# Kernel tuning notes

Hardware: AMD Instinct MI355X
Metric: run time of the kernel (lower is better)

The kernel has to match this reference:

```python
import jax, jax.numpy as jnp
import numpy as np

N = 8192
IN_FEAT = 256
OUT_FEAT = 128
SLOPE = 0.1
NEG_INF = -9e15


def setup_inputs() -> dict:
    key = jax.random.key(0)
    k_doc, k_Ww, k_Wb, k_aw, k_ab = jax.random.split(key, 5)
    doc = jax.random.normal(k_doc, (N, IN_FEAT), dtype=jnp.float32)
    # nn.Linear(inFeat, outFeat): weight [out, in], bias [out]
    W_w = jax.random.normal(k_Ww, (OUT_FEAT, IN_FEAT), dtype=jnp.float32) / np.sqrt(IN_FEAT)
    W_b = jax.random.normal(k_Wb, (OUT_FEAT,), dtype=jnp.float32) * 0.01
    # nn.Linear(2*outFeat, 1): weight [1, 2*out], bias [1]
    a_w = jax.random.normal(k_aw, (1, 2 * OUT_FEAT), dtype=jnp.float32) / np.sqrt(2 * OUT_FEAT)
    a_b = jax.random.normal(k_ab, (1,), dtype=jnp.float32) * 0.01
    return {"doc": doc, "W_w": W_w, "W_b": W_b, "a_w": a_w, "a_b": a_b, "selfLink": 0}


def reference(doc, W_w, W_b, a_w, a_b, selfLink):
    # h = W(doc)  -> [N, outFeat]
    h = doc @ W_w.T + W_b
    n = h.shape[0]
    # Original builds fch[i, j] = concat(h_i, h_j) -> [N, N, 2D] and applies
    # Linear(2D, 1). Algebraically: score[i,j] = h_i . a_src + h_j . a_dst + b,
    # where a_src/a_dst are the two halves of the weight. Same math, O(N*D) mem.
    a_src = a_w[0, :OUT_FEAT]   # [D]
    a_dst = a_w[0, OUT_FEAT:]   # [D]
    s_src = h @ a_src           # [N]
    s_dst = h @ a_dst           # [N]
    att = jax.nn.leaky_relu(s_src[:, None] + s_dst[None, :] + a_b[0], SLOPE)  # [N, N]
    if selfLink == 0:
        # adj = 1 - eye: mask self-edges
        diag = jnp.eye(n, dtype=bool)
        att = jnp.where(diag, NEG_INF, att)
    att = jax.nn.softmax(att, axis=1)
    h_out = jax.nn.leaky_relu(att @ h, SLOPE)  # [N, D]
    return (h_out, att)
```

## Files before the change

kernel.cpp:

```cpp
#include <hip/hip_runtime.h>
#include <math.h>

#define NROW 8192
#define IN_F 256
#define OUT_F 128
#define SLOPE 0.1f
#define SEGS 256
#define SEGROWS 32

typedef float f32x4 __attribute__((ext_vector_type(4)));

__device__ __forceinline__ float lrelu(float x) { return x > 0.f ? x : SLOPE * x; }

__global__ __launch_bounds__(256) void kA_h_s(const float* __restrict__ doc,
                                              const float* __restrict__ Ww,
                                              const float* __restrict__ Wb,
                                              const float* __restrict__ aw,
                                              float* __restrict__ h,
                                              float* __restrict__ s_src,
                                              float* __restrict__ s_dst,
                                              float* __restrict__ E1,
                                              float* __restrict__ E2) {
    __shared__ float4 sdoc[16][64];
    const int t = threadIdx.x;
    const int rowBase = blockIdx.x * 16;
    const float4* doc4 = (const float4*)(doc + (size_t)rowBase * IN_F);
    float4* sflat = &sdoc[0][0];
    for (int i = t; i < 16 * 64; i += 256) sflat[i] = doc4[i];
    __syncthreads();
    const int cq = t & 31;
    const int rg = t >> 5;
    const float4* w0 = (const float4*)(Ww + (size_t)(4 * cq + 0) * IN_F);
    const float4* w1 = (const float4*)(Ww + (size_t)(4 * cq + 1) * IN_F);
    const float4* w2 = (const float4*)(Ww + (size_t)(4 * cq + 2) * IN_F);
    const float4* w3 = (const float4*)(Ww + (size_t)(4 * cq + 3) * IN_F);
    float a00 = 0.f, a01 = 0.f, a02 = 0.f, a03 = 0.f;
    float a10 = 0.f, a11 = 0.f, a12 = 0.f, a13 = 0.f;
#pragma unroll 4
    for (int k = 0; k < 64; ++k) {
        const float4 d0 = sdoc[2 * rg + 0][k];
        const float4 d1 = sdoc[2 * rg + 1][k];
        float4 w;
        w = w0[k];
        a00 += d0.x * w.x + d0.y * w.y + d0.z * w.z + d0.w * w.w;
        a10 += d1.x * w.x + d1.y * w.y + d1.z * w.z + d1.w * w.w;
        w = w1[k];
        a01 += d0.x * w.x + d0.y * w.y + d0.z * w.z + d0.w * w.w;
        a11 += d1.x * w.x + d1.y * w.y + d1.z * w.z + d1.w * w.w;
        w = w2[k];
        a02 += d0.x * w.x + d0.y * w.y + d0.z * w.z + d0.w * w.w;
        a12 += d1.x * w.x + d1.y * w.y + d1.z * w.z + d1.w * w.w;
        w = w3[k];
        a03 += d0.x * w.x + d0.y * w.y + d0.z * w.z + d0.w * w.w;
        a13 += d1.x * w.x + d1.y * w.y + d1.z * w.z + d1.w * w.w;
    }
    const float4 wb4 = ((const float4*)Wb)[cq];
    const float4 as4 = ((const float4*)aw)[cq];
    const float4 ad4 = ((const float4*)(aw + OUT_F))[cq];

#define KA_EPILOG(A0, A1, A2, A3, RR)                                           \
    do {                                                                        \
        float4 hv;                                                              \
        hv.x = (A0) + wb4.x; hv.y = (A1) + wb4.y;                               \
        hv.z = (A2) + wb4.z; hv.w = (A3) + wb4.w;                               \
        const int row = rowBase + 2 * rg + (RR);                                \
        ((float4*)(h + (size_t)row * OUT_F))[cq] = hv;                          \
        float ps = hv.x * as4.x + hv.y * as4.y + hv.z * as4.z + hv.w * as4.w;   \
        float pd = hv.x * ad4.x + hv.y * ad4.y + hv.z * ad4.z + hv.w * ad4.w;   \
        for (int off = 16; off; off >>= 1) {                                    \
            ps += __shfl_down(ps, off, 32);                                     \
            pd += __shfl_down(pd, off, 32);                                     \
        }                                                                       \
        if (cq == 0) {                                                          \
            s_src[row] = ps;                                                    \
            s_dst[row] = pd;                                                    \
            E1[row] = expf(pd);                                                 \
            E2[row] = expf(SLOPE * pd);                                         \
        }                                                                       \
    } while (0)

    KA_EPILOG(a00, a01, a02, a03, 0);
    KA_EPILOG(a10, a11, a12, a13, 1);
#undef KA_EPILOG
}

__global__ __launch_bounds__(256) void kBC_rank_top2(const float* __restrict__ sdst,
                                                     float* __restrict__ red,
                                                     int* __restrict__ perm) {
    const int t = threadIdx.x;
    if (blockIdx.x == SEGS) {
        float m1 = -1e30f, m2 = -1e30f; int i1 = 0;
        for (int j = t; j < NROW; j += 256) {
            const float v = sdst[j];
            if (v > m1) { m2 = m1; m1 = v; i1 = j; }
            else if (v > m2) { m2 = v; }
        }
        __shared__ float sm1[256], sm2[256];
        __shared__ int si[256];
        sm1[t] = m1; sm2[t] = m2; si[t] = i1;
        __syncthreads();
        for (int s = 128; s > 0; s >>= 1) {
            if (t < s) {
                const float om1 = sm1[t + s], om2 = sm2[t + s];
                const int oi = si[t + s];
                if (om1 > sm1[t]) {
                    sm2[t] = fmaxf(sm1[t], om2);
                    sm1[t] = om1; si[t] = oi;
                } else {
                    sm2[t] = fmaxf(sm2[t], om1);
                }
            }
            __syncthreads();
        }
        if (t == 0) { red[0] = sm1[0]; red[1] = sm2[0]; red[2] = __int_as_float(si[0]); }
    } else {
        __shared__ float sd[NROW];
        {
            float4* sd4 = (float4*)sd;
            const float4* g4 = (const float4*)sdst;
            for (int q = t; q < NROW / 4; q += 256) sd4[q] = g4[q];
        }
        __syncthreads();
        const int wave = t >> 6, lane = t & 63;
        const int base = blockIdx.x * 32 + wave * 8;
        float rv[8]; int ri[8]; int cnt[8];
#pragma unroll
        for (int r = 0; r < 8; ++r) { ri[r] = base + r; rv[r] = sd[ri[r]]; cnt[r] = 0; }
        for (int j = lane; j < NROW; j += 64) {
            const float v = sd[j];
#pragma unroll
            for (int r = 0; r < 8; ++r)
                cnt[r] += (v < rv[r] || (v == rv[r] && j < ri[r])) ? 1 : 0;
        }
#pragma unroll
        for (int r = 0; r < 8; ++r)
            for (int off = 32; off; off >>= 1) cnt[r] += __shfl_down(cnt[r], off);
        if (lane == 0) {
#pragma unroll
            for (int r = 0; r < 8; ++r) perm[cnt[r]] = ri[r];
        }
    }
}

__global__ __launch_bounds__(256) void kD_gseg(const int* __restrict__ perm,
                                               const float* __restrict__ E1,
                                               const float* __restrict__ E2,
                                               const float* __restrict__ sdst,
                                               const float* __restrict__ h,
                                               float* __restrict__ sortedS,
                                               float* __restrict__ E1s,
                                               float* __restrict__ E2s,
                                               float* __restrict__ seg1,
                                               float* __restrict__ seg2) {
    __shared__ int sp[SEGROWS];
    __shared__ float se1[SEGROWS], se2[SEGROWS];
    __shared__ float part[2][OUT_F][2];
    const int t = threadIdx.x;
    const int s = blockIdx.x;
    const int r0 = s * SEGROWS;
    if (t < SEGROWS) {
        const int i = perm[r0 + t];
        sp[t] = i;
        const float e1 = E1[i], e2 = E2[i];
        se1[t] = e1; se2[t] = e2;
        sortedS[r0 + t] = sdst[i];
        E1s[r0 + t] = e1;
        E2s[r0 + t] = e2;
    }
    __syncthreads();
    const int c = t & 127;
    const int half = t >> 7;
    float a1 = 0.f, a2 = 0.f;
#pragma unroll
    for (int rr2 = 0; rr2 < 16; ++rr2) {
        const int rr = half * 16 + rr2;
        const float hv = h[(size_t)sp[rr] * OUT_F + c];
        a1 += se1[rr] * hv;
        a2 += se2[rr] * hv;
    }
    part[half][c][0] = a1;
    part[half][c][1] = a2;
    __syncthreads();
    if (t < 128) {
        seg1[(size_t)s * OUT_F + t] = part[0][t][0] + part[1][t][0];
    } else {
        const int c2 = t - 128;
        seg2[(size_t)s * OUT_F + c2] = part[0][c2][1] + part[1][c2][1];
    }
}

__global__ __launch_bounds__(256) void kE_scan(const float* __restrict__ seg1,
                                               const float* __restrict__ seg2,
                                               const float* __restrict__ E1s,
                                               const float* __restrict__ E2s,
                                               float* __restrict__ segUo,
                                               float* __restrict__ segVo,
                                               float* __restrict__ Psuf,
                                               float* __restrict__ Qpre) {
    const int p = blockIdx.x;
    const int t = threadIdx.x;
    if (p < 256) {
        const int arr = p >> 7;
        const int col = p & 127;
        const float* src = arr ? seg2 : seg1;
        const float x = src[(size_t)t * OUT_F + col];
        __shared__ float buf[256];
        const int j = arr ? t : (255 - t);
        buf[j] = x;
        __syncthreads();
        for (int off = 1; off < 256; off <<= 1) {
            const float add = (j >= off) ? buf[j - off] : 0.f;
            __syncthreads();
            buf[j] += add;
            __syncthreads();
        }
        const float excl = buf[j] - x;
        float* dst = arr ? segVo : segUo;
        dst[(size_t)t * OUT_F + col] = excl;
    } else if (p == 256) {
        __shared__ float pp[256];
        const int r0 = t * 32;
        float a = 0.f;
        for (int rr = 0; rr < 32; ++rr) a += E1s[r0 + rr];
        pp[t] = a;
        __syncthreads();
        float off = 0.f;
        for (int t2 = t + 1; t2 < 256; ++t2) off += pp[t2];
        float run = off;
        for (int rr = 31; rr >= 0; --rr) { run += E1s[r0 + rr]; Psuf[r0 + rr] = run; }
        if (t == 0) Psuf[NROW] = 0.f;
    } else {
        __shared__ float pp[256];
        const int r0 = t * 32;
        float a = 0.f;
        for (int rr = 0; rr < 32; ++rr) a += E2s[r0 + rr];
        pp[t] = a;
        __syncthreads();
        float off = 0.f;
        for (int t2 = 0; t2 < t; ++t2) off += pp[t2];
        float rv = off;
        for (int rr = 0; rr < 32; ++rr) { Qpre[r0 + rr] = rv; rv += E2s[r0 + rr]; }
        if (t == 255) Qpre[NROW] = rv;
    }
}

__global__ __launch_bounds__(256) void kF_uv(const int* __restrict__ perm,
                                             const float* __restrict__ h,
                                             const float* __restrict__ E1s,
                                             const float* __restrict__ E2s,
                                             const float* __restrict__ segUo,
                                             const float* __restrict__ segVo,
                                             float* __restrict__ U,
                                             float* __restrict__ V) {
    __shared__ int sp[SEGROWS];
    __shared__ float se1[SEGROWS], se2[SEGROWS];
    __shared__ float sUo[OUT_F], sVo[OUT_F];
    const int t = threadIdx.x;
    const int s = blockIdx.x;
    const int r0 = s * SEGROWS;
    if (t < 128) sUo[t] = segUo[(size_t)s * OUT_F + t];
    else         sVo[t - 128] = segVo[(size_t)s * OUT_F + (t - 128)];
    if (t < SEGROWS) {
        sp[t] = perm[r0 + t];
        se1[t] = E1s[r0 + t];
        se2[t] = E2s[r0 + t];
    }
    __syncthreads();
    const int c = t & 127;
    const int doV = t >> 7;
    float xv[SEGROWS];
#pragma unroll
    for (int rr = 0; rr < SEGROWS; ++rr)
        xv[rr] = h[(size_t)sp[rr] * OUT_F + c];
    if (!doV) {
        float run = sUo[c];
#pragma unroll
        for (int rr = SEGROWS - 1; rr >= 0; --rr) {
            run += se1[rr] * xv[rr];
            U[(size_t)(r0 + rr) * OUT_F + c] = run;
        }
        if (s == SEGS - 1) U[(size_t)NROW * OUT_F + c] = 0.f;
    } else {
        float rv = sVo[c];
#pragma unroll
        for (int rr = 0; rr < SEGROWS; ++rr) {
            V[(size_t)(r0 + rr) * OUT_F + c] = rv;
            rv += se2[rr] * xv[rr];
        }
        if (s == SEGS - 1) V[(size_t)NROW * OUT_F + c] = rv;
    }
}

__global__ __launch_bounds__(256) void kG_hout(const float* __restrict__ s_src,
                                               const float* __restrict__ sdst,
                                               const float* __restrict__ sortedS,
                                               const float* __restrict__ Psuf,
                                               const float* __restrict__ Qpre,
                                               const float* __restrict__ red,
                                               const float* __restrict__ ab,
                                               const int* __restrict__ selfLink,
                                               const float* __restrict__ U,
                                               const float* __restrict__ V,
                                               const float* __restrict__ h,
                                               float* __restrict__ A,
                                               float* __restrict__ B,
                                               float* __restrict__ rZ,
                                               float* __restrict__ T,
                                               float* __restrict__ hout) {
    const int t = threadIdx.x;
    const int i = blockIdx.x * 2 + (t >> 7);
    const int c = t & 127;
    const bool mask = (selfLink[0] == 0);
    const float tt = s_src[i] + ab[0];
    const float M1 = red[0], M2 = red[1];
    const int i1 = __float_as_int(red[2]);
    const float M = (mask && i1 == i) ? M2 : M1;
    const float m = lrelu(tt + M);
    const float Ai = expf(tt - m);
    const float Bi = expf(SLOPE * tt - m);
    const float eii = mask ? expf(lrelu(tt + sdst[i]) - m) : 0.f;
    const float thr = -tt;
    int lo = 0, hi = NROW;
    while (lo < hi) {
        const int mid = (lo + hi) >> 1;
        if (sortedS[mid] > thr) hi = mid; else lo = mid + 1;
    }
    const int k = lo;
    const float Z = Ai * Psuf[k] + Bi * Qpre[k] - eii;
    const float rZi = 1.f / Z;
    const float val = Ai * U[(size_t)k * OUT_F + c] + Bi * V[(size_t)k * OUT_F + c]
                    - eii * h[(size_t)i * OUT_F + c];
    hout[(size_t)i * OUT_F + c] = lrelu(val * rZi);
    if (c == 0) { A[i] = Ai; B[i] = Bi; rZ[i] = rZi; T[i] = tt; }
}

#define RH 16
__global__ __launch_bounds__(256) void kH_att(const float* __restrict__ sdst,
                                              const float* __restrict__ E1,
                                              const float* __restrict__ E2,
                                              const float* __restrict__ A,
                                              const float* __restrict__ B,
                                              const float* __restrict__ rZ,
                                              const float* __restrict__ T,
                                              const int* __restrict__ selfLink,
                                              float* __restrict__ att) {
    __shared__ float rA[RH], rB[RH], rT[RH];
    const int t = threadIdx.x;
    const int rowBase = blockIdx.x * RH;
    if (t < RH) {
        const int i = rowBase + t;
        const float z = rZ[i];
        rA[t] = A[i] * z;
        rB[t] = B[i] * z;
        rT[t] = -T[i];
    }
    __syncthreads();
    const bool mask = (selfLink[0] == 0);
    const f32x4* s4p = (const f32x4*)sdst;
    const f32x4* e1p = (const f32x4*)E1;
    const f32x4* e2p = (const f32x4*)E2;
    for (int it = 0; it < NROW / (4 * 256); ++it) {
        const int q = it * 256 + t;
        const f32x4 s4 = s4p[q];
        const f32x4 e1 = e1p[q];
        const f32x4 e2 = e2p[q];
        const int j0 = q * 4;
#pragma unroll
        for (int r = 0; r < RH; ++r) {
            const float a = rA[r], b = rB[r], thr = rT[r];
            f32x4 o;
            o.x = s4.x > thr ? a * e1.x : b * e2.x;
            o.y = s4.y > thr ? a * e1.y : b * e2.y;
            o.z = s4.z > thr ? a * e1.z : b * e2.z;
            o.w = s4.w > thr ? a * e1.w : b * e2.w;
            const int i = rowBase + r;
            const int d = i - j0;
            if (mask && ((unsigned)d < 4u)) {
                if (d == 0) o.x = 0.f;
                else if (d == 1) o.y = 0.f;
                else if (d == 2) o.z = 0.f;
                else o.w = 0.f;
            }
            __builtin_nontemporal_store(o, (f32x4*)(att + (size_t)i * NROW) + q);
        }
    }
}

extern "C" void kernel_launch(void* const* d_in, const int* in_sizes, int n_in,
                              void* d_out, int out_size, void* d_ws, size_t ws_size,
                              hipStream_t stream) {
    const float* doc = (const float*)d_in[0];
    const float* Ww  = (const float*)d_in[1];
    const float* Wb  = (const float*)d_in[2];
    const float* aw  = (const float*)d_in[3];
    const float* ab  = (const float*)d_in[4];
    const int* selfLink = (const int*)d_in[5];

    float* out  = (float*)d_out;
    float* hout = out;
    float* att  = out + (size_t)NROW * OUT_F;

    float* h = att;
    float* U = att + 1048576;
    float* V = att + 1048576 + 1048704;

    float* ws = (float*)d_ws;
    float* s_src   = ws;
    float* s_dst   = ws + 8192;
    float* E1      = ws + 16384;
    float* E2      = ws + 24576;
    float* sortedS = ws + 32768;
    float* E1s     = ws + 40960;
    float* E2s     = ws + 49152;
    float* Aarr    = ws + 57344;
    float* Barr    = ws + 65536;
    float* rZ      = ws + 73728;
    float* Tarr    = ws + 81920;
    int*   perm    = (int*)(ws + 90112);
    float* seg1    = ws + 98304;
    float* seg2    = ws + 131072;
    float* segUo   = ws + 163840;
    float* segVo   = ws + 196608;
    float* Psuf    = ws + 229376;
    float* Qpre    = ws + 237632;
    float* red     = ws + 245888;

    kA_h_s       <<<512,  256, 0, stream>>>(doc, Ww, Wb, aw, h, s_src, s_dst, E1, E2);
    kBC_rank_top2<<<257,  256, 0, stream>>>(s_dst, red, perm);
    kD_gseg      <<<256,  256, 0, stream>>>(perm, E1, E2, s_dst, h, sortedS, E1s, E2s, seg1, seg2);
    kE_scan      <<<258,  256, 0, stream>>>(seg1, seg2, E1s, E2s, segUo, segVo, Psuf, Qpre);
    kF_uv        <<<256,  256, 0, stream>>>(perm, h, E1s, E2s, segUo, segVo, U, V);
    kG_hout      <<<4096, 256, 0, stream>>>(s_src, s_dst, sortedS, Psuf, Qpre, red, ab, selfLink,
                                            U, V, h, Aarr, Barr, rZ, Tarr, hout);
    kH_att       <<<512,  256, 0, stream>>>(s_dst, E1, E2, Aarr, Barr, rZ, Tarr, selfLink, att);
}
```

Measured before the change: 426.0 us.

## Fuse hout and attention-write kernels, moving h/U/V scratch into workspace

Adds a fused kernel that computes each 16-row block's softmax scalars once (binary search over sortedS staged in shared memory), writes hout, and then streams the attention rows. h, U and V move from the att output buffer into the workspace when it is large enough, so the fused kernel does not overwrite its own inputs. The att stores also drop from nontemporal to ordinary stores. This saves one launch and the A/B/rZ/T round trip, at the cost of a 32KB shared-memory copy per block. The fused path runs only if ws_size is big enough.

Result: faster. 415.3 us (-2.5%).

```diff
diff --git a/kernel.cpp b/kernel.cpp
--- a/kernel.cpp
+++ b/kernel.cpp
@@ -291,6 +291,106 @@
     }
 }
 
+#define RH 16
+__global__ __launch_bounds__(256) void kGH_hout_att(const float* __restrict__ s_src,
+                                                    const float* __restrict__ sdst,
+                                                    const float* __restrict__ sortedS,
+                                                    const float* __restrict__ Psuf,
+                                                    const float* __restrict__ Qpre,
+                                                    const float* __restrict__ red,
+                                                    const float* __restrict__ ab,
+                                                    const int* __restrict__ selfLink,
+                                                    const float* __restrict__ U,
+                                                    const float* __restrict__ V,
+                                                    const float* __restrict__ h,
+                                                    const float* __restrict__ E1,
+                                                    const float* __restrict__ E2,
+                                                    float* __restrict__ hout,
+                                                    float* __restrict__ att) {
+    __shared__ float sS[NROW];
+    __shared__ float sAi[RH], sBi[RH], srZ[RH], seii[RH];
+    __shared__ int   sk[RH];
+    __shared__ float rA[RH], rB[RH], rT[RH];
+    const int t = threadIdx.x;
+    const int rowBase = blockIdx.x * RH;
+    {
+        f32x4* d = (f32x4*)sS;
+        const f32x4* s = (const f32x4*)sortedS;
+        for (int q = t; q < NROW / 4; q += 256) d[q] = s[q];
+    }
+    __syncthreads();
+    if (t < RH) {
+        const int i = rowBase + t;
+        const bool mask = (selfLink[0] == 0);
+        const float tt = s_src[i] + ab[0];
+        const float M1 = red[0], M2 = red[1];
+        const int i1 = __float_as_int(red[2]);
+        const float M = (mask && i1 == i) ? M2 : M1;
+        const float m = lrelu(tt + M);
+        const float Ai = expf(tt - m);
+        const float Bi = expf(SLOPE * tt - m);
+        const float eii = mask ? expf(lrelu(tt + sdst[i]) - m) : 0.f;
+        const float thr = -tt;
+        int lo = 0, hi = NROW;
+        while (lo < hi) {
+            const int mid = (lo + hi) >> 1;
+            if (sS[mid] > thr) hi = mid; else lo = mid + 1;
+        }
+        const int k = lo;
+        const float Z = Ai * Psuf[k] + Bi * Qpre[k] - eii;
+        const float rZi = 1.f / Z;
+        sAi[t] = Ai; sBi[t] = Bi; srZ[t] = rZi; seii[t] = eii; sk[t] = k;
+        rA[t] = Ai * rZi; rB[t] = Bi * rZi; rT[t] = thr;
+    }
+    __syncthreads();
+    {
+        const int c = t & 127;
+        const int half = t >> 7;
+#pragma unroll
+        for (int rp = 0; rp < RH / 2; ++rp) {
+            const int r = rp * 2 + half;
+            const int i = rowBase + r;
+            const int k = sk[r];
+            const float val = sAi[r] * U[(size_t)k * OUT_F + c]
+                            + sBi[r] * V[(size_t)k * OUT_F + c]
+                            - seii[r] * h[(size_t)i * OUT_F + c];
+            hout[(size_t)i * OUT_F + c] = lrelu(val * srZ[r]);
+        }
+    }
+    float cA[RH], cB[RH], cT[RH];
+#pragma unroll
+    for (int r = 0; r < RH; ++r) { cA[r] = rA[r]; cB[r] = rB[r]; cT[r] = rT[r]; }
+    const bool mask = (selfLink[0] == 0);
+    const f32x4* s4p = (const f32x4*)sdst;
+    const f32x4* e1p = (const f32x4*)E1;
+    const f32x4* e2p = (const f32x4*)E2;
+    for (int it = 0; it < NROW / (4 * 256); ++it) {
+        const int q = it * 256 + t;
+        const f32x4 s4 = s4p[q];
+        const f32x4 e1 = e1p[q];
+        const f32x4 e2 = e2p[q];
+        const int j0 = q * 4;
+#pragma unroll
+        for (int r = 0; r < RH; ++r) {
+            const float a = cA[r], b = cB[r], thr = cT[r];
+            f32x4 o;
+            o.x = s4.x > thr ? a * e1.x : b * e2.x;
+            o.y = s4.y > thr ? a * e1.y : b * e2.y;
+            o.z = s4.z > thr ? a * e1.z : b * e2.z;
+            o.w = s4.w > thr ? a * e1.w : b * e2.w;
+            const int i = rowBase + r;
+            const int d = i - j0;
+            if (mask && ((unsigned)d < 4u)) {
+                if (d == 0) o.x = 0.f;
+                else if (d == 1) o.y = 0.f;
+                else if (d == 2) o.z = 0.f;
+                else o.w = 0.f;
+            }
+            *((f32x4*)(att + (size_t)i * NROW) + q) = o;
+        }
+    }
+}
+
 __global__ __launch_bounds__(256) void kG_hout(const float* __restrict__ s_src,
                                                const float* __restrict__ sdst,
                                                const float* __restrict__ sortedS,
@@ -334,7 +434,6 @@
     if (c == 0) { A[i] = Ai; B[i] = Bi; rZ[i] = rZi; T[i] = tt; }
 }
 
-#define RH 16
 __global__ __launch_bounds__(256) void kH_att(const float* __restrict__ sdst,
                                               const float* __restrict__ E1,
                                               const float* __restrict__ E2,
@@ -381,7 +480,7 @@
                 else if (d == 2) o.z = 0.f;
                 else o.w = 0.f;
             }
-            __builtin_nontemporal_store(o, (f32x4*)(att + (size_t)i * NROW) + q);
+            *((f32x4*)(att + (size_t)i * NROW) + q) = o;
         }
     }
 }
@@ -399,10 +498,6 @@
     float* out  = (float*)d_out;
     float* hout = out;
     float* att  = out + (size_t)NROW * OUT_F;
-
-    float* h = att;
-    float* U = att + 1048576;
-    float* V = att + 1048576 + 1048704;
 
     float* ws = (float*)d_ws;
     float* s_src   = ws;
@@ -425,12 +520,34 @@
     float* Qpre    = ws + 237632;
     float* red     = ws + 245888;
 
-    kA_h_s       <<<512,  256, 0, stream>>>(doc, Ww, Wb, aw, h, s_src, s_dst, E1, E2);
-    kBC_rank_top2<<<257,  256, 0, stream>>>(s_dst, red, perm);
-    kD_gseg      <<<256,  256, 0, stream>>>(perm, E1, E2, s_dst, h, sortedS, E1s, E2s, seg1, seg2);
-    kE_scan      <<<258,  256, 0, stream>>>(seg1, seg2, E1s, E2s, segUo, segVo, Psuf, Qpre);
-    kF_uv        <<<256,  256, 0, stream>>>(perm, h, E1s, E2s, segUo, segVo, U, V);
-    kG_hout      <<<4096, 256, 0, stream>>>(s_src, s_dst, sortedS, Psuf, Qpre, red, ab, selfLink,
-                                            U, V, h, Aarr, Barr, rZ, Tarr, hout);
-    kH_att       <<<512,  256, 0, stream>>>(s_dst, E1, E2, Aarr, Barr, rZ, Tarr, selfLink, att);
-}
+    const size_t hN  = (size_t)NROW * OUT_F;
+    const size_t uvN = (size_t)(NROW + 1) * OUT_F;
+    const size_t bigBase = 245952;
+    const size_t neededBytes = (bigBase + hN + 2 * uvN) * sizeof(float);
+    const bool fused = (ws_size >= neededBytes);
+
+    float *h, *U, *V;
+    if (fused) {
+        h = ws + bigBase;
+        U = h + hN;
+        V = U + uvN;
+    } else {
+        h = att;
+        U = att + hN;
+        V = U + uvN;
+    }
+
+    kA_h_s       <<<512, 256, 0, stream>>>(doc, Ww, Wb, aw, h, s_src, s_dst, E1, E2);
+    kBC_rank_top2<<<257, 256, 0, stream>>>(s_dst, red, perm);
+    kD_gseg      <<<256, 256, 0, stream>>>(perm, E1, E2, s_dst, h, sortedS, E1s, E2s, seg1, seg2);
+    kE_scan      <<<258, 256, 0, stream>>>(seg1, seg2, E1s, E2s, segUo, segVo, Psuf, Qpre);
+    kF_uv        <<<256, 256, 0, stream>>>(perm, h, E1s, E2s, segUo, segVo, U, V);
+    if (fused) {
+        kGH_hout_att<<<512, 256, 0, stream>>>(s_src, s_dst, sortedS, Psuf, Qpre, red, ab,
+                                              selfLink, U, V, h, E1, E2, hout, att);
+    } else {
+        kG_hout<<<4096, 256, 0, stream>>>(s_src, s_dst, sortedS, Psuf, Qpre, red, ab, selfLink,
+                                          U, V, h, Aarr, Barr, rZ, Tarr, hout);
+        kH_att <<<512,  256, 0, stream>>>(s_dst, E1, E2, Aarr, Barr, rZ, Tarr, selfLink, att);
+    }
+}
```
